# Kernel tuning notes

Hardware: AMD Instinct MI355X
Metric: run time of the kernel (lower is better)

## Reference

```python
import jax, jax.numpy as jnp
import numpy as np

# --- FineRMoE routing constants (match init_kwargs) ---
TOP_K = 4
G_I, G_O = 2, 2
R_I, R_O = 4, 2
NUM_EXPERTS = 32  # must equal R_O*G_O*R_I*G_I


def _finermoe_router(scores):
    """scores: [T, E]. Returns (probs [T,top_k], selected [T,top_k])."""
    T, E = scores.shape
    S = E // (R_O * G_O)  # experts per concat-shard == R_I*G_I
    cs = scores.reshape(T, R_O * G_O, S)
    # top_k//G_O experts within each (R_O*G_O) shard
    _, add_idx = jax.lax.top_k(cs, TOP_K // G_O)
    add_mask = jnp.any(jax.nn.one_hot(add_idx, S, dtype=bool), axis=-2)  # [T, RO*GO, S]
    # keep the max-scoring R_O shard within each G_O group (argmax -> first max, like torch)
    shard_sum = cs.sum(-1).reshape(T, G_O, R_O)
    concat_mask = jax.nn.one_hot(jnp.argmax(shard_sum, axis=-1), R_O, dtype=bool)
    concat_mask = concat_mask.reshape(T, G_O * R_O)  # flat order matches RO*GO shard dim
    final_mask = (add_mask & concat_mask[:, :, None]).reshape(T, E)
    masked = jnp.where(final_mask, scores, -jnp.inf)
    probs, sel = jax.lax.top_k(masked, TOP_K)
    return probs, sel


def setup_inputs() -> dict:
    key = jax.random.key(0)
    ks = jax.random.split(key, 6)
    B, Sq, H, E, I = 1, 2048, 1024, NUM_EXPERTS, 256
    O = H // G_O  # expert output width
    return {
        "hidden_states": jax.random.normal(ks[0], (B, Sq, H), dtype=jnp.float32),
        "Wr": jax.random.normal(ks[1], (H, E), dtype=jnp.float32) * 0.02,
        "Wg": jax.random.normal(ks[2], (E, H, I), dtype=jnp.float32) * 0.02,
        "Wu": jax.random.normal(ks[3], (E, H, I), dtype=jnp.float32) * 0.02,
        "Wd": jax.random.normal(ks[4], (E, I, O), dtype=jnp.float32) * 0.02,
        "Wc": jax.random.normal(ks[5], (H, H), dtype=jnp.float32) * 0.02,
    }


def reference(hidden_states, Wr, Wg, Wu, Wd, Wc):
    B, Sq, H = hidden_states.shape
    T = B * Sq
    E = Wr.shape[1]
    x = hidden_states.reshape(T, H)
    router_logits = x @ Wr  # [T, E]
    probs, sel = _finermoe_router(router_logits)
    rw = jax.nn.softmax(probs.astype(jnp.float32), axis=1)
    rw = rw / rw.sum(-1, keepdims=True)  # norm_topk_prob
    rw = rw.astype(x.dtype)
    # dense combine weights [T, E] (zero for unselected experts)
    C = jnp.zeros((T, E), x.dtype).at[jnp.arange(T)[:, None], sel].add(rw)
    # all-expert MLP (stacked GEMMs); combine weights mask out unselected tokens
    h = jax.nn.silu(jnp.einsum('th,ehi->eti', x, Wg)) * jnp.einsum('th,ehi->eti', x, Wu)
    y = jnp.einsum('eti,eio->eto', h, Wd)  # [E, T, H//G_O]
    P = E // G_O  # experts per concat shard slice == R_O*G_I*R_I
    out = jnp.einsum('tgp,gpto->tgo', C.reshape(T, G_O, P),
                     y.reshape(G_O, P, T, H // G_O)).reshape(T, H)
    out = out @ Wc  # moe_concat_proj
    return out.reshape(B, Sq, H), router_logits
```

## Files before the change

### kernel.cpp

```cpp
#include <hip/hip_runtime.h>
#include <hip/hip_bf16.h>
#include <math.h>
#include <stdint.h>

typedef __hip_bfloat16 hbf16;

#define T_TOK 2048
#define H_DIM 1024
#define E_NUM 32
#define I_DIM 256
#define O_DIM 512
#define CAP   2048
#define TT    16
#define WT    16
#define XSTR2 520
#define HSTR  264
#define CSTR  32

typedef __bf16 bf16x8 __attribute__((ext_vector_type(8)));
typedef float  f32x4  __attribute__((ext_vector_type(4)));

__device__ __forceinline__ float b2f(hbf16 v) { return __bfloat162float(v); }
__device__ __forceinline__ float bb2f(ushort u) { return __uint_as_float((uint32_t)u << 16); }

__device__ __forceinline__ ushort f2b(float f) {
    uint32_t u = __float_as_uint(f);
    return (ushort)((u + 0x7FFFu + ((u >> 16) & 1u)) >> 16);
}

template<int BF>
__device__ __forceinline__ float ld(const void* p, size_t i) {
    if (BF) return b2f(((const hbf16*)p)[i]);
    else    return ((const float*)p)[i];
}

__device__ __forceinline__ f32x4 mfma_bf16(bf16x8 a, bf16x8 b, f32x4 c) {
    return __builtin_amdgcn_mfma_f32_16x16x32_bf16(a, b, c, 0, 0, 0);
}

__device__ __forceinline__ void sched_fence() { __builtin_amdgcn_sched_barrier(0); }

__global__ __launch_bounds__(256) void detect_kernel(
    const uint32_t* __restrict__ xw, int* __restrict__ flag, int* __restrict__ counts)
{
    __shared__ int cnt;
    if (threadIdx.x == 0) cnt = 0;
    if (threadIdx.x < E_NUM) counts[threadIdx.x * CSTR] = 0;
    __syncthreads();
    int c = 0;
    for (int i = threadIdx.x; i < 1024; i += 256) {
        int e = (xw[i] >> 7) & 0xFF;
        if (e >= 110 && e <= 140) c++;
    }
    atomicAdd(&cnt, c);
    __syncthreads();
    if (threadIdx.x == 0) *flag = (cnt > 512) ? 1 : 0;
}


__device__ void conv3_tile(const void* __restrict__ src, ushort* __restrict__ dst,
                           int bf, int K, int N, int b, float* __restrict__ sh)
{
    int tilesN = N >> 7, tilesK = K >> 5;
    int e  = b / (tilesK * tilesN);
    int r  = b % (tilesK * tilesN);
    int k0 = (r / tilesN) << 5;
    int n0 = (r % tilesN) << 7;
    size_t base = (size_t)e * K * N;
    int tid = threadIdx.x;
    {
        int row = tid >> 3, c0 = (tid & 7) * 16;
        if (!bf) {
            const float* sp = (const float*)src + base + (size_t)(k0 + row) * N + n0 + c0;
            #pragma unroll
            for (int i = 0; i < 4; ++i) {
                float4 v = *(const float4*)(sp + i * 4);
                sh[row * 132 + c0 + i*4 + 0] = v.x;
                sh[row * 132 + c0 + i*4 + 1] = v.y;
                sh[row * 132 + c0 + i*4 + 2] = v.z;
                sh[row * 132 + c0 + i*4 + 3] = v.w;
            }
        } else {
            const hbf16* sp = (const hbf16*)src + base + (size_t)(k0 + row) * N + n0 + c0;
            #pragma unroll
            for (int i = 0; i < 16; ++i) sh[row * 132 + c0 + i] = b2f(sp[i]);
        }
    }
    __syncthreads();
    {
        int nn = tid >> 1, kk = (tid & 1) * 16;
        union { ushort v[16]; uint4 u[2]; } R;
        #pragma unroll
        for (int i = 0; i < 16; ++i) R.v[i] = f2b(sh[(kk + i) * 132 + nn]);
        ushort* dp = dst + base + ((size_t)(k0 >> 5) * N + (n0 + nn)) * 32 + kk;
        *(uint4*)dp       = R.u[0];
        *(uint4*)(dp + 8) = R.u[1];
    }
    __syncthreads();
}

template<int BF>
__device__ void router3_body(const void* __restrict__ x, const void* __restrict__ Wr,
                             void* __restrict__ out_base,
                             int* __restrict__ counts, int* __restrict__ tok_list,
                             float* __restrict__ wt_list,
                             float* __restrict__ xs, float* __restrict__ sl,
                             float* __restrict__ sf, int t0)
{
    int tid  = threadIdx.x;
    int e    = tid & 31;
    int half = tid >> 5;

    {
        int t = tid >> 7;
        int c = (tid & 127) * 8;
        if (!BF) {
            const float* xp = (const float*)x + (size_t)(t0 + t) * H_DIM + c;
            *(float4*)&xs[t*1024 + c]     = *(const float4*)xp;
            *(float4*)&xs[t*1024 + c + 4] = *(const float4*)(xp + 4);
        } else {
            const hbf16* xp = (const hbf16*)x + (size_t)(t0 + t) * H_DIM + c;
            #pragma unroll
            for (int j = 0; j < 8; ++j) xs[t*1024 + c + j] = b2f(xp[j]);
        }
    }
    __syncthreads();

    float a0 = 0.f, a1 = 0.f;
    int kbase = half * 128;
    const float* xr0 = &xs[kbase];
    const float* xr1 = &xs[1024 + kbase];
    #pragma unroll 8
    for (int k = 0; k < 128; ++k) {
        float w = ld<BF>(Wr, (size_t)(kbase + k) * E_NUM + e);
        a0 = fmaf(xr0[k], w, a0);
        a1 = fmaf(xr1[k], w, a1);
    }
    sl[(0*8 + half)*32 + e] = a0;
    sl[(1*8 + half)*32 + e] = a1;
    __syncthreads();

    if (tid < 64) {
        int t  = tid >> 5;
        int ee = tid & 31;
        float s = 0.f;
        #pragma unroll
        for (int h = 0; h < 8; ++h) s += sl[(t*8 + h)*32 + ee];
        sf[t*32 + ee] = s;
        size_t li = (size_t)T_TOK * H_DIM + (size_t)(t0 + t) * E_NUM + ee;
        if (BF) ((hbf16*)out_base)[li] = __float2bfloat16(s);
        else    ((float*)out_base)[li] = s;
    }
    __syncthreads();

    if (tid < 2) {
        int t = t0 + tid;
        float s[E_NUM];
        #pragma unroll
        for (int i = 0; i < E_NUM; ++i) s[i] = sf[tid * 32 + i];

        int   selE[4];
        float selL[4];
        int ns = 0;
        for (int g = 0; g < 2; ++g) {
            float sum0 = 0.f, sum1 = 0.f;
            #pragma unroll
            for (int j = 0; j < 8; ++j) {
                sum0 += s[(2*g)   * 8 + j];
                sum1 += s[(2*g+1) * 8 + j];
            }
            int bestSh = (sum1 > sum0) ? (2*g+1) : (2*g);
            int base = bestSh * 8;
            int i1 = 0;
            for (int j = 1; j < 8; ++j) if (s[base+j] > s[base+i1]) i1 = j;
            int i2 = -1;
            for (int j = 0; j < 8; ++j) {
                if (j == i1) continue;
                if (i2 < 0 || s[base+j] > s[base+i2]) i2 = j;
            }
            selE[ns] = base + i1; selL[ns] = s[base+i1]; ++ns;
            selE[ns] = base + i2; selL[ns] = s[base+i2]; ++ns;
        }
        float m = fmaxf(fmaxf(selL[0], selL[1]), fmaxf(selL[2], selL[3]));
        float w[4];
        float sum = 0.f;
        for (int j = 0; j < 4; ++j) { w[j] = expf(selL[j] - m); sum += w[j]; }
        float inv = 1.f / sum;
        for (int j = 0; j < 4; ++j) {
            int ee = selE[j];
            int pos = atomicAdd(&counts[ee * CSTR], 1);
            if (pos >= 0 && pos < CAP) {
                tok_list[ee * CAP + pos] = t | (j << 11);
                wt_list[ee * CAP + pos]  = w[j] * inv;
            }
        }
    }
}

__global__ __launch_bounds__(256) void fused_cr_kernel(
    const void* x, const void* Wr,
    const void* Wg, const void* Wu, const void* Wd, const void* Wc,
    ushort* Wg_t, ushort* Wu_t, ushort* Wd_t, ushort* Wc_t,
    void* out_base, const int* __restrict__ flag,
    int* counts, int* tok_list, float* wt_list)
{
    __shared__ __align__(16) float sh[32 * 132];
    int b = blockIdx.x;
    if (b < 1024) {
        float* xs = sh;
        float* sl = sh + 2048;
        float* sf = sh + 2560;
        if (*flag) router3_body<1>(x, Wr, out_base, counts, tok_list, wt_list,
                                   xs, sl, sf, b * 2);
        else       router3_body<0>(x, Wr, out_base, counts, tok_list, wt_list,
                                   xs, sl, sf, b * 2);
    } else {
        int bb = b - 1024;
        int bf = *flag;
        if      (bb < 2048) conv3_tile(Wg, Wg_t, bf, 1024,  256, bb,        sh);
        else if (bb < 4096) conv3_tile(Wu, Wu_t, bf, 1024,  256, bb - 2048, sh);
        else if (bb < 5120) conv3_tile(Wd, Wd_t, bf,  256,  512, bb - 4096, sh);
        else                conv3_tile(Wc, Wc_t, bf, 1024, 1024, bb - 5120, sh);
    }
}

template<int BF>
__device__ void expert3_body(const void* __restrict__ x,
    const ushort* __restrict__ Wg_t, const ushort* __restrict__ Wu_t,
    const ushort* __restrict__ Wd_t,
    const int* __restrict__ counts, const int* __restrict__ tok_list,
    const float* __restrict__ wt_list, ushort* __restrict__ ybuf,
    ushort* __restrict__ xA, ushort* __restrict__ hsm,
    int* __restrict__ tokid, float* __restrict__ twt, int* __restrict__ tslot)
{
    int e = blockIdx.x;
    int n = counts[e * CSTR]; n = n < 0 ? 0 : (n > CAP ? CAP : n);
    int t0 = blockIdx.y * 32;
    if (t0 >= n) return;
    int tid  = threadIdx.x;
    int lane = tid & 63, wv = tid >> 6;
    int q = lane >> 4, l15 = lane & 15;

    if (tid < 32) {
        int it = t0 + tid;
        int id; float ww;
        if (it < n) { id = tok_list[e*CAP + it]; ww = wt_list[e*CAP + it]; }
        else        { id = tok_list[e*CAP + t0]; ww = 0.f; }
        tokid[tid] = id & 2047;
        tslot[tid] = (id >> 11) & 3;
        twt[tid]   = ww;
    }
    __syncthreads();

    const ushort* Bg0 = Wg_t + (size_t)e * (H_DIM * I_DIM) + (wv*32 + l15) * 32 + q*8;
    const ushort* Bu0 = Wu_t + (size_t)e * (H_DIM * I_DIM) + (wv*32 + l15) * 32 + q*8;

    f32x4 Cg[2][2], Cu[2][2];
    #pragma unroll
    for (int m = 0; m < 2; ++m)
        #pragma unroll
        for (int j = 0; j < 2; ++j) { Cg[m][j] = (f32x4)0.f; Cu[m][j] = (f32x4)0.f; }

    bf16x8 bg[3][4][2], bu[3][4][2];
    #pragma unroll
    for (int p = 0; p < 2; ++p)
        #pragma unroll
        for (int ig = 0; ig < 4; ++ig)
            #pragma unroll
            for (int j = 0; j < 2; ++j) {
                int idx = p * 4 + ig;
                bg[p][ig][j] = *(const bf16x8*)(Bg0 + (size_t)idx*8192 + j*512);
                bu[p][ig][j] = *(const bf16x8*)(Bu0 + (size_t)idx*8192 + j*512);
            }
    sched_fence();

    #pragma unroll
    for (int hk = 0; hk < 2; ++hk) {
        if (hk) __syncthreads();

        {
            int row = tid >> 4;
            int kb  = (tid & 15) * 8;
            size_t srow = (size_t)tokid[row] * H_DIM + hk * 512;
            #pragma unroll
            for (int c = 0; c < 4; ++c) {
                int k = kb + c * 128;
                union { ushort v[8]; uint4 u; } U;
                if (BF) {
                    U.u = *(const uint4*)((const ushort*)x + srow + k);
                } else {
                    const float* xp = (const float*)x + srow + k;
                    float4 a = *(const float4*)xp;
                    float4 b = *(const float4*)(xp + 4);
                    U.v[0]=f2b(a.x); U.v[1]=f2b(a.y); U.v[2]=f2b(a.z); U.v[3]=f2b(a.w);
                    U.v[4]=f2b(b.x); U.v[5]=f2b(b.y); U.v[6]=f2b(b.z); U.v[7]=f2b(b.w);
                }
                *(uint4*)&xA[row * XSTR2 + k] = U.u;
            }
        }
        __syncthreads();

        #pragma unroll
        for (int g2 = 0; g2 < 4; ++g2) {
            int grp = hk * 4 + g2;
            int pf  = grp + 2;
            if (pf < 8) {
                int pb = pf % 3;
                #pragma unroll
                for (int ig = 0; ig < 4; ++ig)
                    #pragma unroll
                    for (int j = 0; j < 2; ++j) {
                        int idx = pf * 4 + ig;
                        bg[pb][ig][j] = *(const bf16x8*)(Bg0 + (size_t)idx*8192 + j*512);
                        bu[pb][ig][j] = *(const bf16x8*)(Bu0 + (size_t)idx*8192 + j*512);
                    }
            }
            sched_fence();
            int cb = grp % 3;
            #pragma unroll
            for (int ig = 0; ig < 4; ++ig) {
                int kl = (g2 * 4 + ig) * 32;
                bf16x8 A0 = *(const bf16x8*)&xA[(l15)      * XSTR2 + kl + q*8];
                bf16x8 A1 = *(const bf16x8*)&xA[(16 + l15) * XSTR2 + kl + q*8];
                #pragma unroll
                for (int j = 0; j < 2; ++j) {
                    Cg[0][j] = mfma_bf16(A0, bg[cb][ig][j], Cg[0][j]);
                    Cg[1][j] = mfma_bf16(A1, bg[cb][ig][j], Cg[1][j]);
                    Cu[0][j] = mfma_bf16(A0, bu[cb][ig][j], Cu[0][j]);
                    Cu[1][j] = mfma_bf16(A1, bu[cb][ig][j], Cu[1][j]);
                }
            }
        }
    }

    const ushort* Bd0 = Wd_t + (size_t)e * (I_DIM * O_DIM) + (wv*64 + l15) * 32 + q*8;
    bf16x8 bd[2][4][4];
    #pragma unroll
    for (int g2 = 0; g2 < 2; ++g2)
        #pragma unroll
        for (int kc2 = 0; kc2 < 4; ++kc2)
            #pragma unroll
            for (int j = 0; j < 4; ++j)
                bd[g2][kc2][j] = *(const bf16x8*)(Bd0 + (size_t)(g2*4 + kc2)*16384 + j*512);
    sched_fence();

    #pragma unroll
    for (int m = 0; m < 2; ++m)
        #pragma unroll
        for (int j = 0; j < 2; ++j)
            #pragma unroll
            for (int r = 0; r < 4; ++r) {
                float g = Cg[m][j][r], u = Cu[m][j][r];
                float h = (g / (1.f + expf(-g))) * u;
                hsm[(m*16 + q*4 + r) * HSTR + wv*32 + j*16 + l15] = f2b(h);
            }
    __syncthreads();

    f32x4 Cd[2][4];
    #pragma unroll
    for (int m = 0; m < 2; ++m)
        #pragma unroll
        for (int j = 0; j < 4; ++j) Cd[m][j] = (f32x4)0.f;

    #pragma unroll
    for (int g2 = 0; g2 < 2; ++g2)
        #pragma unroll
        for (int kc2 = 0; kc2 < 4; ++kc2) {
            int kc = g2 * 4 + kc2;
            bf16x8 A0 = *(const bf16x8*)&hsm[(l15)      * HSTR + kc*32 + q*8];
            bf16x8 A1 = *(const bf16x8*)&hsm[(16 + l15) * HSTR + kc*32 + q*8];
            #pragma unroll
            for (int j = 0; j < 4; ++j) {
                Cd[0][j] = mfma_bf16(A0, bd[g2][kc2][j], Cd[0][j]);
                Cd[1][j] = mfma_bf16(A1, bd[g2][kc2][j], Cd[1][j]);
            }
        }

    #pragma unroll
    for (int m = 0; m < 2; ++m)
        #pragma unroll
        for (int r = 0; r < 4; ++r) {
            int row = m*16 + q*4 + r;
            if (t0 + row < n) {
                float ww = twt[row];
                size_t base = ((size_t)tokid[row] * 4 + tslot[row]) * O_DIM;
                #pragma unroll
                for (int j = 0; j < 4; ++j)
                    ybuf[base + wv*64 + j*16 + l15] = f2b(ww * Cd[m][j][r]);
            }
        }
}

__global__ __launch_bounds__(512, 2) void expert3_kernel(
    const void* x, const ushort* Wg_t, const ushort* Wu_t, const ushort* Wd_t,
    const int* flag, const int* counts, const int* tok_list, const float* wt_list,
    ushort* ybuf)
{
    __shared__ ushort xA[32 * XSTR2];
    __shared__ ushort hsm[32 * HSTR];
    __shared__ int    tokid[32];
    __shared__ float  twt[32];
    __shared__ int    tslot[32];
    if (*flag) expert3_body<1>(x, Wg_t, Wu_t, Wd_t, counts, tok_list, wt_list,
                               ybuf, xA, hsm, tokid, twt, tslot);
    else       expert3_body<0>(x, Wg_t, Wu_t, Wd_t, counts, tok_list, wt_list,
                               ybuf, xA, hsm, tokid, twt, tslot);
}

template<int BF>
__device__ void wc3_body(const ushort* __restrict__ ybuf, const ushort* __restrict__ Wc_t,
                         void* __restrict__ out_base, ushort* __restrict__ zA)
{
    int m0  = blockIdx.x * 32;
    int n0  = blockIdx.y * 256;
    int tid = threadIdx.x;
    int lane = tid & 63, wv = tid >> 6;
    int q = lane >> 4, l15 = lane & 15;

    const ushort* Bc0 = Wc_t + (size_t)(n0 + wv*16 + l15) * 32 + q*8;
    f32x4 C[2];
    C[0] = (f32x4)0.f; C[1] = (f32x4)0.f;

    bf16x8 bc[3][4];
    #pragma unroll
    for (int p = 0; p < 2; ++p)
        #pragma unroll
        for (int ig = 0; ig < 4; ++ig)
            bc[p][ig] = *(const bf16x8*)(Bc0 + (size_t)(p*4 + ig)*32768);
    sched_fence();

    #pragma unroll
    for (int hk = 0; hk < 2; ++hk) {
        if (hk) __syncthreads();

        {
            int row = tid >> 5;
            int kb  = (tid & 31) * 8;
            int t = m0 + row;
            int s0 = hk ? 2 : 0;
            #pragma unroll
            for (int c = 0; c < 2; ++c) {
                int hl = kb + c * 256;
                const ushort* p0 = ybuf + ((size_t)t * 4 + s0) * O_DIM + hl;
                union { ushort v[8]; uint4 u; } A, B, R;
                A.u = *(const uint4*)p0;
                B.u = *(const uint4*)(p0 + O_DIM);
                #pragma unroll
                for (int i = 0; i < 8; ++i) R.v[i] = f2b(bb2f(A.v[i]) + bb2f(B.v[i]));
                *(uint4*)&zA[row * XSTR2 + hl] = R.u;
            }
        }
        __syncthreads();

        #pragma unroll
        for (int g2 = 0; g2 < 4; ++g2) {
            int grp = hk * 4 + g2;
            int pf  = grp + 2;
            if (pf < 8) {
                int pb = pf % 3;
                #pragma unroll
                for (int ig = 0; ig < 4; ++ig)
                    bc[pb][ig] = *(const bf16x8*)(Bc0 + (size_t)(pf*4 + ig)*32768);
            }
            sched_fence();
            int cb = grp % 3;
            #pragma unroll
            for (int ig = 0; ig < 4; ++ig) {
                int kl = (g2 * 4 + ig) * 32;
                bf16x8 A0 = *(const bf16x8*)&zA[(l15)      * XSTR2 + kl + q*8];
                bf16x8 A1 = *(const bf16x8*)&zA[(16 + l15) * XSTR2 + kl + q*8];
                C[0] = mfma_bf16(A0, bc[cb][ig], C[0]);
                C[1] = mfma_bf16(A1, bc[cb][ig], C[1]);
            }
        }
    }

    #pragma unroll
    for (int m = 0; m < 2; ++m)
        #pragma unroll
        for (int r = 0; r < 4; ++r) {
            int row = m0 + m*16 + q*4 + r;
            int col = n0 + wv*16 + l15;
            size_t o = (size_t)row * H_DIM + col;
            if (BF) ((hbf16*)out_base)[o] = __float2bfloat16(C[m][r]);
            else    ((float*)out_base)[o] = C[m][r];
        }
}

__global__ __launch_bounds__(1024, 4) void wc3_kernel(
    const ushort* ybuf, const ushort* Wc_t, void* out_base, const int* flag)
{
    __shared__ ushort zA[32 * XSTR2];
    if (*flag) wc3_body<1>(ybuf, Wc_t, out_base, zA);
    else       wc3_body<0>(ybuf, Wc_t, out_base, zA);
}


__global__ __launch_bounds__(256) void zero_kernel(
    float* __restrict__ z_fp32, float* __restrict__ z_bf16,
    const int* __restrict__ flag, int* __restrict__ counts)
{
    float* base = (*flag) ? z_bf16 : z_fp32;
    size_t i = (size_t)blockIdx.x * 256 + threadIdx.x;
    ((float4*)base)[i] = make_float4(0.f, 0.f, 0.f, 0.f);
    if (blockIdx.x == 0 && threadIdx.x < E_NUM) ((int*)counts)[threadIdx.x * CSTR] = 0;
}

template<int BF>
__device__ void router_body(const void* __restrict__ x, const void* __restrict__ Wr,
                            void* __restrict__ out_base,
                            int* __restrict__ counts, int* __restrict__ tok_list,
                            float* __restrict__ wt_list, float* __restrict__ sl)
{
    int t    = blockIdx.x;
    int lane = threadIdx.x;
    int e    = lane & 31;
    int half = lane >> 5;

    float acc = 0.f;
    size_t xoff = (size_t)t * H_DIM;
    int h0 = half * (H_DIM / 2);
    for (int h = h0; h < h0 + H_DIM / 2; ++h)
        acc = fmaf(ld<BF>(x, xoff + h), ld<BF>(Wr, (size_t)h * E_NUM + e), acc);
    acc += __shfl_down(acc, 32);

    if (lane < 32) {
        sl[e] = acc;
        size_t li = (size_t)T_TOK * H_DIM + (size_t)t * E_NUM + e;
        if (BF) ((hbf16*)out_base)[li] = __float2bfloat16(acc);
        else    ((float*)out_base)[li] = acc;
    }
    __syncthreads();

    if (lane == 0) {
        float s[E_NUM];
        #pragma unroll
        for (int i = 0; i < E_NUM; ++i) s[i] = sl[i];
        int   selE[4];
        float selL[4];
        int ns = 0;
        for (int g = 0; g < 2; ++g) {
            float sum0 = 0.f, sum1 = 0.f;
            #pragma unroll
            for (int j = 0; j < 8; ++j) {
                sum0 += s[(2*g)   * 8 + j];
                sum1 += s[(2*g+1) * 8 + j];
            }
            int bestSh = (sum1 > sum0) ? (2*g+1) : (2*g);
            int base = bestSh * 8;
            int i1 = 0;
            for (int j = 1; j < 8; ++j) if (s[base+j] > s[base+i1]) i1 = j;
            int i2 = -1;
            for (int j = 0; j < 8; ++j) {
                if (j == i1) continue;
                if (i2 < 0 || s[base+j] > s[base+i2]) i2 = j;
            }
            selE[ns] = base + i1; selL[ns] = s[base+i1]; ++ns;
            selE[ns] = base + i2; selL[ns] = s[base+i2]; ++ns;
        }
        float m = fmaxf(fmaxf(selL[0], selL[1]), fmaxf(selL[2], selL[3]));
        float w[4];
        float sum = 0.f;
        for (int j = 0; j < 4; ++j) { w[j] = expf(selL[j] - m); sum += w[j]; }
        float inv = 1.f / sum;
        for (int j = 0; j < 4; ++j) {
            int ee = selE[j];
            int pos = atomicAdd(&counts[ee * CSTR], 1);
            if (pos >= 0 && pos < CAP) {
                tok_list[ee * CAP + pos] = t;
                wt_list[ee * CAP + pos]  = w[j] * inv;
            }
        }
    }
}

__global__ __launch_bounds__(64) void router_kernel(
    const void* x, const void* Wr, void* out_base, const int* flag,
    int* counts, int* tok_list, float* wt_list)
{
    __shared__ float sl[E_NUM];
    if (*flag) router_body<1>(x, Wr, out_base, counts, tok_list, wt_list, sl);
    else       router_body<0>(x, Wr, out_base, counts, tok_list, wt_list, sl);
}

template<int BF>
__device__ void expert_body(const void* __restrict__ x,
                            const void* __restrict__ Wg, const void* __restrict__ Wu,
                            const void* __restrict__ Wd,
                            const int* __restrict__ counts, const int* __restrict__ tok_list,
                            const float* __restrict__ wt_list,
                            float* __restrict__ z, float* __restrict__ xsbuf)
{
    int e = blockIdx.x;
    int n = counts[e * CSTR];
    n = n < 0 ? 0 : (n > CAP ? CAP : n);
    int t0 = blockIdx.y * TT;
    if (t0 >= n) return;
    int tid = threadIdx.x;

    float (*xs)[H_DIM] = reinterpret_cast<float(*)[H_DIM]>(xsbuf);
    float (*hs)[I_DIM] = reinterpret_cast<float(*)[I_DIM]>(xsbuf);

    const int*   tl = tok_list + e * CAP;
    const float* wl = wt_list  + e * CAP;

    for (int idx = tid; idx < TT * H_DIM; idx += 256) {
        int tt = idx >> 10;
        int h  = idx & (H_DIM - 1);
        int it = t0 + tt;
        int tkn = (it < n) ? tl[it] : tl[t0];
        tkn = (tkn < 0) ? 0 : (tkn >= T_TOK ? T_TOK - 1 : tkn);
        xs[tt][h] = ld<BF>(x, (size_t)tkn * H_DIM + h);
    }
    __syncthreads();

    size_t wbase = (size_t)e * H_DIM * I_DIM + tid;
    float ag[TT], au[TT];
    #pragma unroll
    for (int tt = 0; tt < TT; ++tt) { ag[tt] = 0.f; au[tt] = 0.f; }

    for (int k = 0; k < H_DIM; k += 4) {
        float g0 = ld<BF>(Wg, wbase + (size_t)(k+0) * I_DIM);
        float g1 = ld<BF>(Wg, wbase + (size_t)(k+1) * I_DIM);
        float g2 = ld<BF>(Wg, wbase + (size_t)(k+2) * I_DIM);
        float g3 = ld<BF>(Wg, wbase + (size_t)(k+3) * I_DIM);
        float u0 = ld<BF>(Wu, wbase + (size_t)(k+0) * I_DIM);
        float u1 = ld<BF>(Wu, wbase + (size_t)(k+1) * I_DIM);
        float u2 = ld<BF>(Wu, wbase + (size_t)(k+2) * I_DIM);
        float u3 = ld<BF>(Wu, wbase + (size_t)(k+3) * I_DIM);
        #pragma unroll
        for (int tt = 0; tt < TT; ++tt) {
            float4 xv = *(const float4*)&xs[tt][k];
            ag[tt] = fmaf(xv.w, g3, fmaf(xv.z, g2, fmaf(xv.y, g1, fmaf(xv.x, g0, ag[tt]))));
            au[tt] = fmaf(xv.w, u3, fmaf(xv.z, u2, fmaf(xv.y, u1, fmaf(xv.x, u0, au[tt]))));
        }
    }
    float hval[TT];
    #pragma unroll
    for (int tt = 0; tt < TT; ++tt) {
        float g = ag[tt];
        hval[tt] = (g / (1.f + expf(-g))) * au[tt];
    }
    __syncthreads();
    #pragma unroll
    for (int tt = 0; tt < TT; ++tt) hs[tt][tid] = hval[tt];
    __syncthreads();

    size_t dbase = (size_t)e * I_DIM * O_DIM;
    float y0[TT], y1[TT];
    #pragma unroll
    for (int tt = 0; tt < TT; ++tt) { y0[tt] = 0.f; y1[tt] = 0.f; }

    for (int k = 0; k < I_DIM; k += 4) {
        float d00 = ld<BF>(Wd, dbase + (size_t)(k+0) * O_DIM + tid);
        float d01 = ld<BF>(Wd, dbase + (size_t)(k+1) * O_DIM + tid);
        float d02 = ld<BF>(Wd, dbase + (size_t)(k+2) * O_DIM + tid);
        float d03 = ld<BF>(Wd, dbase + (size_t)(k+3) * O_DIM + tid);
        float d10 = ld<BF>(Wd, dbase + (size_t)(k+0) * O_DIM + tid + 256);
        float d11 = ld<BF>(Wd, dbase + (size_t)(k+1) * O_DIM + tid + 256);
        float d12 = ld<BF>(Wd, dbase + (size_t)(k+2) * O_DIM + tid + 256);
        float d13 = ld<BF>(Wd, dbase + (size_t)(k+3) * O_DIM + tid + 256);
        #pragma unroll
        for (int tt = 0; tt < TT; ++tt) {
            float4 hv = *(const float4*)&hs[tt][k];
            y0[tt] = fmaf(hv.w, d03, fmaf(hv.z, d02, fmaf(hv.y, d01, fmaf(hv.x, d00, y0[tt]))));
            y1[tt] = fmaf(hv.w, d13, fmaf(hv.z, d12, fmaf(hv.y, d11, fmaf(hv.x, d10, y1[tt]))));
        }
    }

    int gsel = e >> 4;
    size_t colbase = (size_t)gsel * O_DIM;
    #pragma unroll
    for (int tt = 0; tt < TT; ++tt) {
        int it = t0 + tt;
        if (it < n) {
            float w  = wl[it];
            int tkn = tl[it];
            tkn = (tkn < 0) ? 0 : (tkn >= T_TOK ? T_TOK - 1 : tkn);
            atomicAdd(&z[(size_t)tkn * H_DIM + colbase + tid],       w * y0[tt]);
            atomicAdd(&z[(size_t)tkn * H_DIM + colbase + tid + 256], w * y1[tt]);
        }
    }
}

__global__ __launch_bounds__(256) void expert_kernel(
    const void* x, const void* Wg, const void* Wu, const void* Wd,
    const int* flag, const int* counts, const int* tok_list, const float* wt_list,
    float* z_fp32, float* z_bf16)
{
    __shared__ __align__(16) float xsbuf[TT * H_DIM];
    if (*flag) expert_body<1>(x, Wg, Wu, Wd, counts, tok_list, wt_list, z_bf16, xsbuf);
    else       expert_body<0>(x, Wg, Wu, Wd, counts, tok_list, wt_list, z_fp32, xsbuf);
}

template<int BF>
__device__ void wc_body(const float* __restrict__ z, const void* __restrict__ Wc,
                        void* __restrict__ out_base, float* __restrict__ psbuf)
{
    int t0  = blockIdx.x * WT;
    int tid = threadIdx.x;
    float (*ps)[H_DIM] = reinterpret_cast<float(*)[H_DIM]>(psbuf);

    for (int idx = tid; idx < WT * H_DIM; idx += 256) {
        int tt = idx >> 10;
        int h  = idx & (H_DIM - 1);
        ps[tt][h] = z[(size_t)(t0 + tt) * H_DIM + h];
    }
    __syncthreads();

    float acc[WT][4];
    #pragma unroll
    for (int tt = 0; tt < WT; ++tt)
        #pragma unroll
        for (int qq = 0; qq < 4; ++qq) acc[tt][qq] = 0.f;

    for (int k = 0; k < H_DIM; k += 2) {
        float c00 = ld<BF>(Wc, (size_t)(k+0) * H_DIM + tid);
        float c01 = ld<BF>(Wc, (size_t)(k+0) * H_DIM + tid + 256);
        float c02 = ld<BF>(Wc, (size_t)(k+0) * H_DIM + tid + 512);
        float c03 = ld<BF>(Wc, (size_t)(k+0) * H_DIM + tid + 768);
        float c10 = ld<BF>(Wc, (size_t)(k+1) * H_DIM + tid);
        float c11 = ld<BF>(Wc, (size_t)(k+1) * H_DIM + tid + 256);
        float c12 = ld<BF>(Wc, (size_t)(k+1) * H_DIM + tid + 512);
        float c13 = ld<BF>(Wc, (size_t)(k+1) * H_DIM + tid + 768);
        #pragma unroll
        for (int tt = 0; tt < WT; ++tt) {
            float2 pv = *(const float2*)&ps[tt][k];
            acc[tt][0] = fmaf(pv.y, c10, fmaf(pv.x, c00, acc[tt][0]));
            acc[tt][1] = fmaf(pv.y, c11, fmaf(pv.x, c01, acc[tt][1]));
            acc[tt][2] = fmaf(pv.y, c12, fmaf(pv.x, c02, acc[tt][2]));
            acc[tt][3] = fmaf(pv.y, c13, fmaf(pv.x, c03, acc[tt][3]));
        }
    }

    #pragma unroll
    for (int tt = 0; tt < WT; ++tt) {
        #pragma unroll
        for (int qq = 0; qq < 4; ++qq) {
            size_t o = (size_t)(t0 + tt) * H_DIM + tid + 256 * qq;
            if (BF) ((hbf16*)out_base)[o] = __float2bfloat16(acc[tt][qq]);
            else    ((float*)out_base)[o] = acc[tt][qq];
        }
    }
}

__global__ __launch_bounds__(256) void wc_kernel(
    const float* z_fp32, const float* z_bf16, const void* Wc,
    void* out_base, const int* flag)
{
    __shared__ __align__(16) float psbuf[WT * H_DIM];
    if (*flag) wc_body<1>(z_bf16, Wc, out_base, psbuf);
    else       wc_body<0>(z_fp32, Wc, out_base, psbuf);
}

extern "C" void kernel_launch(void* const* d_in, const int* in_sizes, int n_in,
                              void* d_out, int out_size, void* d_ws, size_t ws_size,
                              hipStream_t stream)
{
    (void)in_sizes; (void)n_in; (void)out_size;

    const void* x  = d_in[0];
    const void* Wr = d_in[1];
    const void* Wg = d_in[2];
    const void* Wu = d_in[3];
    const void* Wd = d_in[4];
    const void* Wc = d_in[5];

    char* ws = (char*)d_ws;
    int*   counts   = (int*)(ws + 0);
    int*   flag     = (int*)(ws + 4096);
    int*   tok_list = (int*)(ws + 8192);
    float* wt_list  = (float*)(ws + 8192 + (size_t)E_NUM * CAP * 4);

    detect_kernel<<<1, 256, 0, stream>>>((const uint32_t*)x, flag, counts);

    if (ws_size >= ((size_t)58 << 20)) {
        ushort* ybuf = (ushort*)(ws + ((size_t)1  << 20));
        ushort* Wg_t = (ushort*)(ws + ((size_t)16 << 20));
        ushort* Wu_t = (ushort*)(ws + ((size_t)32 << 20));
        ushort* Wd_t = (ushort*)(ws + ((size_t)48 << 20));
        ushort* Wc_t = (ushort*)(ws + ((size_t)56 << 20));

        fused_cr_kernel<<<1024 + 5376, 256, 0, stream>>>(
            x, Wr, Wg, Wu, Wd, Wc, Wg_t, Wu_t, Wd_t, Wc_t,
            d_out, flag, counts, tok_list, wt_list);
        expert3_kernel<<<dim3(E_NUM, T_TOK / 32), 512, 0, stream>>>(
            x, Wg_t, Wu_t, Wd_t, flag, counts, tok_list, wt_list, ybuf);
        wc3_kernel<<<dim3(T_TOK / 32, 4), 1024, 0, stream>>>(ybuf, Wc_t, d_out, flag);
    } else {
        float* z_bf16 = (float*)(ws + (1u << 20));
        float* z_fp32 = (float*)d_out;
        zero_kernel<<<T_TOK, 256, 0, stream>>>(z_fp32, z_bf16, flag, counts);
        router_kernel<<<T_TOK, 64, 0, stream>>>(x, Wr, d_out, flag, counts, tok_list, wt_list);
        expert_kernel<<<dim3(E_NUM, T_TOK / TT), 256, 0, stream>>>(
            x, Wg, Wu, Wd, flag, counts, tok_list, wt_list, z_fp32, z_bf16);
        wc_kernel<<<T_TOK / WT, 256, 0, stream>>>(z_fp32, z_bf16, Wc, d_out, flag);
    }
}
```

Before: 210.3 us.

## Stage expert weights through double-buffered LDS with cooperative coalesced loads

The expert kernel used to have each wave load its own Wg/Wu/Wd fragments straight from global memory into registers, using a 3-deep register prefetch. It now has all 512 threads load contiguous weight chunks together and write them into a double-buffered LDS tile; the MFMAs read B fragments from LDS, with a barrier per K-step. The aim is to make global loads coalesced and to drop the large per-thread register arrays, which could help occupancy. In exchange it adds 64KB of LDS per block, which may limit blocks per CU under launch_bounds(512,2), and adds 40 barriers per block. The Wc projection kernel's register prefetch is also reduced from triple to double buffering.

```diff
diff --git a/kernel.cpp b/kernel.cpp
--- a/kernel.cpp
+++ b/kernel.cpp
@@ -230,7 +230,7 @@
     const ushort* __restrict__ Wd_t,
     const int* __restrict__ counts, const int* __restrict__ tok_list,
     const float* __restrict__ wt_list, ushort* __restrict__ ybuf,
-    ushort* __restrict__ xA, ushort* __restrict__ hsm,
+    ushort* __restrict__ xA, ushort* __restrict__ hsm, ushort* __restrict__ wls,
     int* __restrict__ tokid, float* __restrict__ twt, int* __restrict__ tslot)
 {
     int e = blockIdx.x;
@@ -252,8 +252,13 @@
     }
     __syncthreads();
 
-    const ushort* Bg0 = Wg_t + (size_t)e * (H_DIM * I_DIM) + (wv*32 + l15) * 32 + q*8;
-    const ushort* Bu0 = Wu_t + (size_t)e * (H_DIM * I_DIM) + (wv*32 + l15) * 32 + q*8;
+    const ushort* WgE = Wg_t + (size_t)e * (H_DIM * I_DIM);
+    const ushort* WuE = Wu_t + (size_t)e * (H_DIM * I_DIM);
+    const ushort* WdE = Wd_t + (size_t)e * (I_DIM * O_DIM);
+
+    int wt = tid & 255;
+    const ushort* gsel = (tid < 256) ? WgE : WuE;
+    int lsel = (tid < 256) ? 0 : 8192;
 
     f32x4 Cg[2][2], Cu[2][2];
     #pragma unroll
@@ -261,27 +266,46 @@
         #pragma unroll
         for (int j = 0; j < 2; ++j) { Cg[m][j] = (f32x4)0.f; Cu[m][j] = (f32x4)0.f; }
 
-    bf16x8 bg[3][4][2], bu[3][4][2];
-    #pragma unroll
-    for (int p = 0; p < 2; ++p)
-        #pragma unroll
-        for (int ig = 0; ig < 4; ++ig)
-            #pragma unroll
-            for (int j = 0; j < 2; ++j) {
-                int idx = p * 4 + ig;
-                bg[p][ig][j] = *(const bf16x8*)(Bg0 + (size_t)idx*8192 + j*512);
-                bu[p][ig][j] = *(const bf16x8*)(Bu0 + (size_t)idx*8192 + j*512);
-            }
+    uint4 st[4];
+
+    #pragma unroll
+    for (int c = 0; c < 4; ++c)
+        st[c] = *(const uint4*)(gsel + (c*256 + wt)*8);
     sched_fence();
-
-    #pragma unroll
-    for (int hk = 0; hk < 2; ++hk) {
-        if (hk) __syncthreads();
-
-        {
+    {
+        int row = tid >> 4;
+        int kb  = (tid & 15) * 8;
+        size_t srow = (size_t)tokid[row] * H_DIM;
+        #pragma unroll
+        for (int c = 0; c < 4; ++c) {
+            int k = kb + c * 128;
+            union { ushort v[8]; uint4 u; } U;
+            if (BF) {
+                U.u = *(const uint4*)((const ushort*)x + srow + k);
+            } else {
+                const float* xp = (const float*)x + srow + k;
+                float4 a = *(const float4*)xp;
+                float4 b = *(const float4*)(xp + 4);
+                U.v[0]=f2b(a.x); U.v[1]=f2b(a.y); U.v[2]=f2b(a.z); U.v[3]=f2b(a.w);
+                U.v[4]=f2b(b.x); U.v[5]=f2b(b.y); U.v[6]=f2b(b.z); U.v[7]=f2b(b.w);
+            }
+            *(uint4*)&xA[row * XSTR2 + k] = U.u;
+        }
+    }
+    __syncthreads();
+    {
+        ushort* dst = wls + lsel;
+        #pragma unroll
+        for (int c = 0; c < 4; ++c)
+            *(uint4*)&dst[(c*256 + wt)*8] = st[c];
+    }
+    __syncthreads();
+
+    for (int idx = 0; idx < 32; ++idx) {
+        if (idx == 16) {
             int row = tid >> 4;
             int kb  = (tid & 15) * 8;
-            size_t srow = (size_t)tokid[row] * H_DIM + hk * 512;
+            size_t srow = (size_t)tokid[row] * H_DIM + 512;
             #pragma unroll
             for (int c = 0; c < 4; ++c) {
                 int k = kb + c * 128;
@@ -297,53 +321,44 @@
                 }
                 *(uint4*)&xA[row * XSTR2 + k] = U.u;
             }
+            __syncthreads();
+        }
+        if (idx < 31) {
+            size_t gb = (size_t)(idx + 1) * 8192;
+            #pragma unroll
+            for (int c = 0; c < 4; ++c)
+                st[c] = *(const uint4*)(gsel + gb + (c*256 + wt)*8);
+        }
+        sched_fence();
+        {
+            const ushort* wgb = wls + (idx & 1) * 16384;
+            int kl = (idx & 15) * 32;
+            bf16x8 A0 = *(const bf16x8*)&xA[(l15)      * XSTR2 + kl + q*8];
+            bf16x8 A1 = *(const bf16x8*)&xA[(16 + l15) * XSTR2 + kl + q*8];
+            #pragma unroll
+            for (int j = 0; j < 2; ++j) {
+                int off = (wv*32 + j*16 + l15) * 32 + q*8;
+                bf16x8 bgf = *(const bf16x8*)&wgb[off];
+                bf16x8 buf2 = *(const bf16x8*)&wgb[8192 + off];
+                Cg[0][j] = mfma_bf16(A0, bgf, Cg[0][j]);
+                Cg[1][j] = mfma_bf16(A1, bgf, Cg[1][j]);
+                Cu[0][j] = mfma_bf16(A0, buf2, Cu[0][j]);
+                Cu[1][j] = mfma_bf16(A1, buf2, Cu[1][j]);
+            }
+        }
+        if (idx < 31) {
+            ushort* dst = wls + ((idx + 1) & 1) * 16384 + lsel;
+            #pragma unroll
+            for (int c = 0; c < 4; ++c)
+                *(uint4*)&dst[(c*256 + wt)*8] = st[c];
         }
         __syncthreads();
-
-        #pragma unroll
-        for (int g2 = 0; g2 < 4; ++g2) {
-            int grp = hk * 4 + g2;
-            int pf  = grp + 2;
-            if (pf < 8) {
-                int pb = pf % 3;
-                #pragma unroll
-                for (int ig = 0; ig < 4; ++ig)
-                    #pragma unroll
-                    for (int j = 0; j < 2; ++j) {
-                        int idx = pf * 4 + ig;
-                        bg[pb][ig][j] = *(const bf16x8*)(Bg0 + (size_t)idx*8192 + j*512);
-                        bu[pb][ig][j] = *(const bf16x8*)(Bu0 + (size_t)idx*8192 + j*512);
-                    }
-            }
-            sched_fence();
-            int cb = grp % 3;
-            #pragma unroll
-            for (int ig = 0; ig < 4; ++ig) {
-                int kl = (g2 * 4 + ig) * 32;
-                bf16x8 A0 = *(const bf16x8*)&xA[(l15)      * XSTR2 + kl + q*8];
-                bf16x8 A1 = *(const bf16x8*)&xA[(16 + l15) * XSTR2 + kl + q*8];
-                #pragma unroll
-                for (int j = 0; j < 2; ++j) {
-                    Cg[0][j] = mfma_bf16(A0, bg[cb][ig][j], Cg[0][j]);
-                    Cg[1][j] = mfma_bf16(A1, bg[cb][ig][j], Cg[1][j]);
-                    Cu[0][j] = mfma_bf16(A0, bu[cb][ig][j], Cu[0][j]);
-                    Cu[1][j] = mfma_bf16(A1, bu[cb][ig][j], Cu[1][j]);
-                }
-            }
-        }
-    }
-
-    const ushort* Bd0 = Wd_t + (size_t)e * (I_DIM * O_DIM) + (wv*64 + l15) * 32 + q*8;
-    bf16x8 bd[2][4][4];
-    #pragma unroll
-    for (int g2 = 0; g2 < 2; ++g2)
-        #pragma unroll
-        for (int kc2 = 0; kc2 < 4; ++kc2)
-            #pragma unroll
-            for (int j = 0; j < 4; ++j)
-                bd[g2][kc2][j] = *(const bf16x8*)(Bd0 + (size_t)(g2*4 + kc2)*16384 + j*512);
+    }
+
+    #pragma unroll
+    for (int c = 0; c < 4; ++c)
+        st[c] = *(const uint4*)(WdE + (c*512 + tid)*8);
     sched_fence();
-
     #pragma unroll
     for (int m = 0; m < 2; ++m)
         #pragma unroll
@@ -355,6 +370,12 @@
                 hsm[(m*16 + q*4 + r) * HSTR + wv*32 + j*16 + l15] = f2b(h);
             }
     __syncthreads();
+    {
+        #pragma unroll
+        for (int c = 0; c < 4; ++c)
+            *(uint4*)&wls[(c*512 + tid)*8] = st[c];
+    }
+    __syncthreads();
 
     f32x4 Cd[2][4];
     #pragma unroll
@@ -362,19 +383,34 @@
         #pragma unroll
         for (int j = 0; j < 4; ++j) Cd[m][j] = (f32x4)0.f;
 
-    #pragma unroll
-    for (int g2 = 0; g2 < 2; ++g2)
-        #pragma unroll
-        for (int kc2 = 0; kc2 < 4; ++kc2) {
-            int kc = g2 * 4 + kc2;
+    for (int kc = 0; kc < 8; ++kc) {
+        if (kc < 7) {
+            size_t gb = (size_t)(kc + 1) * 16384;
+            #pragma unroll
+            for (int c = 0; c < 4; ++c)
+                st[c] = *(const uint4*)(WdE + gb + (c*512 + tid)*8);
+        }
+        sched_fence();
+        {
+            const ushort* wdb = wls + (kc & 1) * 16384;
             bf16x8 A0 = *(const bf16x8*)&hsm[(l15)      * HSTR + kc*32 + q*8];
             bf16x8 A1 = *(const bf16x8*)&hsm[(16 + l15) * HSTR + kc*32 + q*8];
             #pragma unroll
             for (int j = 0; j < 4; ++j) {
-                Cd[0][j] = mfma_bf16(A0, bd[g2][kc2][j], Cd[0][j]);
-                Cd[1][j] = mfma_bf16(A1, bd[g2][kc2][j], Cd[1][j]);
-            }
-        }
+                int off = (wv*64 + j*16 + l15) * 32 + q*8;
+                bf16x8 bdf = *(const bf16x8*)&wdb[off];
+                Cd[0][j] = mfma_bf16(A0, bdf, Cd[0][j]);
+                Cd[1][j] = mfma_bf16(A1, bdf, Cd[1][j]);
+            }
+        }
+        if (kc < 7) {
+            ushort* dst = wls + ((kc + 1) & 1) * 16384;
+            #pragma unroll
+            for (int c = 0; c < 4; ++c)
+                *(uint4*)&dst[(c*512 + tid)*8] = st[c];
+        }
+        __syncthreads();
+    }
 
     #pragma unroll
     for (int m = 0; m < 2; ++m)
@@ -398,13 +434,14 @@
 {
     __shared__ ushort xA[32 * XSTR2];
     __shared__ ushort hsm[32 * HSTR];
+    __shared__ ushort wls[2 * 16384];
     __shared__ int    tokid[32];
     __shared__ float  twt[32];
     __shared__ int    tslot[32];
     if (*flag) expert3_body<1>(x, Wg_t, Wu_t, Wd_t, counts, tok_list, wt_list,
-                               ybuf, xA, hsm, tokid, twt, tslot);
+                               ybuf, xA, hsm, wls, tokid, twt, tslot);
     else       expert3_body<0>(x, Wg_t, Wu_t, Wd_t, counts, tok_list, wt_list,
-                               ybuf, xA, hsm, tokid, twt, tslot);
+                               ybuf, xA, hsm, wls, tokid, twt, tslot);
 }
 
 template<int BF>
@@ -421,12 +458,10 @@
     f32x4 C[2];
     C[0] = (f32x4)0.f; C[1] = (f32x4)0.f;
 
-    bf16x8 bc[3][4];
-    #pragma unroll
-    for (int p = 0; p < 2; ++p)
-        #pragma unroll
-        for (int ig = 0; ig < 4; ++ig)
-            bc[p][ig] = *(const bf16x8*)(Bc0 + (size_t)(p*4 + ig)*32768);
+    bf16x8 bc[2][4];
+    #pragma unroll
+    for (int ig = 0; ig < 4; ++ig)
+        bc[0][ig] = *(const bf16x8*)(Bc0 + (size_t)ig*32768);
     sched_fence();
 
     #pragma unroll
@@ -455,15 +490,15 @@
         #pragma unroll
         for (int g2 = 0; g2 < 4; ++g2) {
             int grp = hk * 4 + g2;
-            int pf  = grp + 2;
-            if (pf < 8) {
-                int pb = pf % 3;
+            int cb  = grp & 1;
+            if (grp < 7) {
                 #pragma unroll
-                for (int ig = 0; ig < 4; ++ig)
-                    bc[pb][ig] = *(const bf16x8*)(Bc0 + (size_t)(pf*4 + ig)*32768);
+                for (int ig = 0; ig < 4; ++ig) {
+                    int idx = (grp + 1) * 4 + ig;
+                    bc[cb^1][ig] = *(const bf16x8*)(Bc0 + (size_t)idx*32768);
+                }
             }
             sched_fence();
-            int cb = grp % 3;
             #pragma unroll
             for (int ig = 0; ig < 4; ++ig) {
                 int kl = (g2 * 4 + ig) * 32;
```

Result: slower. 284.1 us (+35.1%).
